# Optimization experiments

Measured on AMD Instinct MI355X. Metric: run time of the kernel, lower is better.

## Reference

```python
import jax, jax.numpy as jnp
import numpy as np

E = 16          # ensemble_size
S = 64          # state_size
A = 32          # action_size
R = 1           # reward_size
I = S + A       # combined input size
HS = 64         # SubModel_state hidden
HR = 32         # SubModel_reward hidden
B = 16384       # batch


def setup_inputs() -> dict:
    key = jax.random.key(0)
    ks = jax.random.split(key, 10)

    def init_lin(k, fan_in, shape):
        bound = 1.0 / np.sqrt(fan_in)
        return jax.random.uniform(k, shape, jnp.float32, -bound, bound)

    return {
        "state": jax.random.normal(ks[0], (B, S), jnp.float32),
        "action": jax.random.normal(ks[1], (B, A), jnp.float32),
        # stacked ensemble state-model weights (torch Linear stores [out,in]; we use [in,out])
        "W1": init_lin(ks[2], I, (E, I, HS)),
        "b1": init_lin(ks[3], I, (E, HS)),
        "W2": init_lin(ks[4], HS, (E, HS, S)),
        "b2": init_lin(ks[5], HS, (E, S)),
        # stacked ensemble reward-model weights
        "rW1": init_lin(ks[6], I, (E, I, HR)),
        "rb1": init_lin(ks[7], I, (E, HR)),
        "rW2": init_lin(ks[8], HR, (E, HR, R)),
        "rb2": init_lin(ks[9], HR, (E, R)),
    }


def reference(state, action, W1, b1, W2, b2, rW1, rb1, rW2, rb2):
    x = jnp.concatenate([state, action], axis=1)  # [B, I]
    # state models: Linear -> ReLU -> Linear, all ensemble members in one batched GEMM
    h = jax.nn.relu(jnp.einsum("bi,eih->ebh", x, W1) + b1[:, None, :])  # [E, B, HS]
    pred_states = jnp.einsum("ebh,ehs->ebs", h, W2) + b2[:, None, :]    # [E, B, S]
    # reward models: Linear -> ReLU -> Linear -> clamp(-100, 200)
    hr = jax.nn.relu(jnp.einsum("bi,eih->ebh", x, rW1) + rb1[:, None, :])  # [E, B, HR]
    pred_rewards = jnp.einsum("ebh,ehr->ebr", hr, rW2) + rb2[:, None, :]   # [E, B, R]
    pred_rewards = jnp.clip(pred_rewards, -100.0, 200.0)
    return (pred_states, pred_rewards)
```

## Files before the change

kernel.cpp:

```cpp
#include <hip/hip_runtime.h>
#include <hip/hip_bf16.h>
#include <cstdint>
#include <cstddef>

#define Bsz 16384
#define Esz 16
#define Ssz 64
#define Asz 32
#define Isz 96
#define HSz 64
#define HRz 32

#define NTM 256
#define CHUNK 512
#define NTILE 8
#define NCHUNK 32

typedef __attribute__((ext_vector_type(8))) short bf16x8;
typedef __attribute__((ext_vector_type(4))) short short4v;
typedef __attribute__((ext_vector_type(4))) float f32x4;

static __device__ __forceinline__ short f2bf(float f) {
    __hip_bfloat16 b = __float2bfloat16(f);
    return *reinterpret_cast<short*>(&b);
}
static __device__ __forceinline__ float bf2f(short s) {
    union { uint32_t u; float f; } v; v.u = ((uint32_t)(uint16_t)s) << 16; return v.f;
}
static __device__ __forceinline__ bf16x8 pack8(float4 lo, float4 hi) {
    bf16x8 r;
    r[0] = f2bf(lo.x); r[1] = f2bf(lo.y); r[2] = f2bf(lo.z); r[3] = f2bf(lo.w);
    r[4] = f2bf(hi.x); r[5] = f2bf(hi.y); r[6] = f2bf(hi.z); r[7] = f2bf(hi.w);
    return r;
}

__global__ __launch_bounds__(NTM, 2)
void fused_all(const float* __restrict__ state, const float* __restrict__ action,
               const float* __restrict__ W1, const float* __restrict__ b1,
               const float* __restrict__ W2, const float* __restrict__ b2,
               const float* __restrict__ rW1, const float* __restrict__ rb1,
               const float* __restrict__ rW2, const float* __restrict__ rb2,
               float* __restrict__ outS, float* __restrict__ outR)
{
    __shared__ __align__(16) short HT[4][16][68];

    const int bid = blockIdx.x;
    const int xcd = bid & 7;
    const int rem = bid >> 3;
    const int e   = rem & (Esz - 1);
    const int c0  = (xcd + 8 * (rem >> 4)) * CHUNK;

    const int w = threadIdx.x >> 6, lane = threadIdx.x & 63;
    const int lr = lane & 15, lg = lane >> 4;

    bf16x8 w1r[4][3], rw1r[2][3], w2r[4][2];
    {
        const float* base = W1 + (size_t)e * Isz * HSz;
        #pragma unroll
        for (int nt = 0; nt < 4; ++nt)
            #pragma unroll
            for (int kk = 0; kk < 3; ++kk) {
                const float* p = base + (kk * 32 + lg * 8) * HSz + nt * 16 + lr;
                bf16x8 r;
                #pragma unroll
                for (int t = 0; t < 8; ++t) r[t] = f2bf(p[t * HSz]);
                w1r[nt][kk] = r;
            }
    }
    {
        const float* base = rW1 + (size_t)e * Isz * HRz;
        #pragma unroll
        for (int nt = 0; nt < 2; ++nt)
            #pragma unroll
            for (int kk = 0; kk < 3; ++kk) {
                const float* p = base + (kk * 32 + lg * 8) * HRz + nt * 16 + lr;
                bf16x8 r;
                #pragma unroll
                for (int t = 0; t < 8; ++t) r[t] = f2bf(p[t * HRz]);
                rw1r[nt][kk] = r;
            }
    }
    {
        const float* base = W2 + (size_t)e * HSz * Ssz;
        #pragma unroll
        for (int nt = 0; nt < 4; ++nt)
            #pragma unroll
            for (int kk = 0; kk < 2; ++kk) {
                const float* p = base + (kk * 32 + lg * 8) * Ssz + nt * 16 + lr;
                bf16x8 r;
                #pragma unroll
                for (int t = 0; t < 8; ++t) r[t] = f2bf(p[t * Ssz]);
                w2r[nt][kk] = r;
            }
    }

    short4v b1p[4], b2p[4], rb1p[2], rw2p[2];
    #pragma unroll
    for (int nt = 0; nt < 4; ++nt) {
        float4 v1 = *(const float4*)&b1[e * HSz + nt * 16 + lg * 4];
        float4 v2 = *(const float4*)&b2[e * Ssz + nt * 16 + lg * 4];
        b1p[nt] = (short4v){ f2bf(v1.x), f2bf(v1.y), f2bf(v1.z), f2bf(v1.w) };
        b2p[nt] = (short4v){ f2bf(v2.x), f2bf(v2.y), f2bf(v2.z), f2bf(v2.w) };
    }
    #pragma unroll
    for (int nt = 0; nt < 2; ++nt) {
        float4 v1 = *(const float4*)&rb1[e * HRz + nt * 16 + lg * 4];
        float4 v2 = *(const float4*)&rW2[e * HRz + nt * 16 + lg * 4];
        rb1p[nt] = (short4v){ f2bf(v1.x), f2bf(v1.y), f2bf(v1.z), f2bf(v1.w) };
        rw2p[nt] = (short4v){ f2bf(v2.x), f2bf(v2.y), f2bf(v2.z), f2bf(v2.w) };
    }
    const float rb2s = rb2[e];

    const int row0 = c0 + w * 16 + lr;
    const float* sbase = state  + (size_t)row0 * Ssz + lg * 8;
    const float* abase = action + (size_t)row0 * Asz + lg * 8;

    float4 xs0 = *(const float4*)(sbase);
    float4 xs1 = *(const float4*)(sbase + 4);
    float4 xs2 = *(const float4*)(sbase + 32);
    float4 xs3 = *(const float4*)(sbase + 36);
    float4 xa0 = *(const float4*)(abase);
    float4 xa1 = *(const float4*)(abase + 4);
    bf16x8 a0 = pack8(xs0, xs1);
    bf16x8 a1 = pack8(xs2, xs3);
    bf16x8 a2 = pack8(xa0, xa1);

    #pragma unroll 1
    for (int t = 0; t < NTILE; ++t) {
        const int tn = (t + 1) & (NTILE - 1);
        const float* sp = sbase + (size_t)tn * 64 * Ssz;
        const float* ap = abase + (size_t)tn * 64 * Asz;
        float4 ns0 = *(const float4*)(sp);
        float4 ns1 = *(const float4*)(sp + 4);
        float4 ns2 = *(const float4*)(sp + 32);
        float4 ns3 = *(const float4*)(sp + 36);
        float4 na0 = *(const float4*)(ap);
        float4 na1 = *(const float4*)(ap + 4);

        f32x4 accS[4];
        #pragma unroll
        for (int nt = 0; nt < 4; ++nt) {
            f32x4 acc = (f32x4){ bf2f(b1p[nt][0]), bf2f(b1p[nt][1]),
                                 bf2f(b1p[nt][2]), bf2f(b1p[nt][3]) };
            acc = __builtin_amdgcn_mfma_f32_16x16x32_bf16(w1r[nt][0], a0, acc, 0, 0, 0);
            acc = __builtin_amdgcn_mfma_f32_16x16x32_bf16(w1r[nt][1], a1, acc, 0, 0, 0);
            acc = __builtin_amdgcn_mfma_f32_16x16x32_bf16(w1r[nt][2], a2, acc, 0, 0, 0);
            accS[nt] = acc;
        }
        f32x4 accR[2];
        #pragma unroll
        for (int nt = 0; nt < 2; ++nt) {
            f32x4 acc = (f32x4){ bf2f(rb1p[nt][0]), bf2f(rb1p[nt][1]),
                                 bf2f(rb1p[nt][2]), bf2f(rb1p[nt][3]) };
            acc = __builtin_amdgcn_mfma_f32_16x16x32_bf16(rw1r[nt][0], a0, acc, 0, 0, 0);
            acc = __builtin_amdgcn_mfma_f32_16x16x32_bf16(rw1r[nt][1], a1, acc, 0, 0, 0);
            acc = __builtin_amdgcn_mfma_f32_16x16x32_bf16(rw1r[nt][2], a2, acc, 0, 0, 0);
            accR[nt] = acc;
        }

        #pragma unroll
        for (int nt = 0; nt < 4; ++nt) {
            short4v p = { f2bf(fmaxf(accS[nt][0], 0.f)),
                          f2bf(fmaxf(accS[nt][1], 0.f)),
                          f2bf(fmaxf(accS[nt][2], 0.f)),
                          f2bf(fmaxf(accS[nt][3], 0.f)) };
            *(short4v*)&HT[w][lr][nt * 16 + lg * 4] = p;
        }

        float rp = 0.f;
        #pragma unroll
        for (int nt = 0; nt < 2; ++nt) {
            rp += fmaxf(accR[nt][0], 0.f) * bf2f(rw2p[nt][0]);
            rp += fmaxf(accR[nt][1], 0.f) * bf2f(rw2p[nt][1]);
            rp += fmaxf(accR[nt][2], 0.f) * bf2f(rw2p[nt][2]);
            rp += fmaxf(accR[nt][3], 0.f) * bf2f(rw2p[nt][3]);
        }
        rp += __shfl_xor(rp, 16);
        rp += __shfl_xor(rp, 32);
        if (lane < 16)
            outR[(size_t)e * Bsz + row0 + t * 64] = fminf(fmaxf(rp + rb2s, -100.f), 200.f);

        bf16x8 h0 = *(const bf16x8*)&HT[w][lr][lg * 8];
        bf16x8 h1 = *(const bf16x8*)&HT[w][lr][32 + lg * 8];
        #pragma unroll
        for (int nt = 0; nt < 4; ++nt) {
            f32x4 acc = (f32x4){ bf2f(b2p[nt][0]), bf2f(b2p[nt][1]),
                                 bf2f(b2p[nt][2]), bf2f(b2p[nt][3]) };
            acc = __builtin_amdgcn_mfma_f32_16x16x32_bf16(w2r[nt][0], h0, acc, 0, 0, 0);
            acc = __builtin_amdgcn_mfma_f32_16x16x32_bf16(w2r[nt][1], h1, acc, 0, 0, 0);
            float4 o = { acc[0], acc[1], acc[2], acc[3] };
            *(float4*)&outS[((size_t)e * Bsz + row0 + t * 64) * Ssz + nt * 16 + lg * 4] = o;
        }

        a0 = pack8(ns0, ns1);
        a1 = pack8(ns2, ns3);
        a2 = pack8(na0, na1);
    }
}

extern "C" void kernel_launch(void* const* d_in, const int* in_sizes, int n_in,
                              void* d_out, int out_size, void* d_ws, size_t ws_size,
                              hipStream_t stream) {
    const float* state  = (const float*)d_in[0];
    const float* action = (const float*)d_in[1];
    const float* W1  = (const float*)d_in[2];
    const float* b1  = (const float*)d_in[3];
    const float* W2  = (const float*)d_in[4];
    const float* b2  = (const float*)d_in[5];
    const float* rW1 = (const float*)d_in[6];
    const float* rb1 = (const float*)d_in[7];
    const float* rW2 = (const float*)d_in[8];
    const float* rb2 = (const float*)d_in[9];

    float* outS = (float*)d_out;
    float* outR = outS + (size_t)Esz * Bsz * Ssz;

    fused_all<<<Esz * (Bsz / CHUNK), NTM, 0, stream>>>(
        state, action, W1, b1, W2, b2, rW1, rb1, rW2, rb2, outS, outR);
}
```

Before: 29.13 us.

## Split state and reward models into separate block roles to cut register pressure

Each block now runs either the state MLP or the reward MLP. The grid has 512 state blocks plus 256 reward blocks, each reward block covering 1024 rows. Separating the roles lowers per-thread register demand, and launch bounds rise to 3 blocks per CU to raise occupancy. The cost is that reward blocks re-read state and action inputs from memory that the fused version shared, and the grid gains extra blocks.

```diff
diff --git a/kernel.cpp b/kernel.cpp
--- a/kernel.cpp
+++ b/kernel.cpp
@@ -12,9 +12,12 @@
 #define HRz 32
 
 #define NTM 256
-#define CHUNK 512
-#define NTILE 8
-#define NCHUNK 32
+#define SCHUNK 512
+#define SNTILE 8
+#define NSB 512
+#define RCHUNK 1024
+#define RNTILE 16
+#define NRB 256
 
 typedef __attribute__((ext_vector_type(8))) short bf16x8;
 typedef __attribute__((ext_vector_type(4))) short short4v;
@@ -34,7 +37,7 @@
     return r;
 }
 
-__global__ __launch_bounds__(NTM, 2)
+__global__ __launch_bounds__(NTM, 3)
 void fused_all(const float* __restrict__ state, const float* __restrict__ action,
                const float* __restrict__ W1, const float* __restrict__ b1,
                const float* __restrict__ W2, const float* __restrict__ b2,
@@ -45,156 +48,193 @@
     __shared__ __align__(16) short HT[4][16][68];
 
     const int bid = blockIdx.x;
-    const int xcd = bid & 7;
-    const int rem = bid >> 3;
-    const int e   = rem & (Esz - 1);
-    const int c0  = (xcd + 8 * (rem >> 4)) * CHUNK;
-
     const int w = threadIdx.x >> 6, lane = threadIdx.x & 63;
     const int lr = lane & 15, lg = lane >> 4;
 
-    bf16x8 w1r[4][3], rw1r[2][3], w2r[4][2];
-    {
-        const float* base = W1 + (size_t)e * Isz * HSz;
-        #pragma unroll
-        for (int nt = 0; nt < 4; ++nt)
-            #pragma unroll
-            for (int kk = 0; kk < 3; ++kk) {
-                const float* p = base + (kk * 32 + lg * 8) * HSz + nt * 16 + lr;
-                bf16x8 r;
+    if (bid < NSB) {
+        const int xcd = bid & 7;
+        const int rem = bid >> 3;
+        const int e   = rem & (Esz - 1);
+        const int c0  = (xcd + 8 * (rem >> 4)) * SCHUNK;
+
+        bf16x8 w1r[4][3], w2r[4][2];
+        {
+            const float* base = W1 + (size_t)e * Isz * HSz;
+            #pragma unroll
+            for (int nt = 0; nt < 4; ++nt)
                 #pragma unroll
-                for (int t = 0; t < 8; ++t) r[t] = f2bf(p[t * HSz]);
-                w1r[nt][kk] = r;
-            }
-    }
-    {
-        const float* base = rW1 + (size_t)e * Isz * HRz;
-        #pragma unroll
-        for (int nt = 0; nt < 2; ++nt)
-            #pragma unroll
-            for (int kk = 0; kk < 3; ++kk) {
-                const float* p = base + (kk * 32 + lg * 8) * HRz + nt * 16 + lr;
-                bf16x8 r;
+                for (int kk = 0; kk < 3; ++kk) {
+                    const float* p = base + (kk * 32 + lg * 8) * HSz + nt * 16 + lr;
+                    bf16x8 r;
+                    #pragma unroll
+                    for (int t = 0; t < 8; ++t) r[t] = f2bf(p[t * HSz]);
+                    w1r[nt][kk] = r;
+                }
+        }
+        {
+            const float* base = W2 + (size_t)e * HSz * Ssz;
+            #pragma unroll
+            for (int nt = 0; nt < 4; ++nt)
                 #pragma unroll
-                for (int t = 0; t < 8; ++t) r[t] = f2bf(p[t * HRz]);
-                rw1r[nt][kk] = r;
-            }
-    }
-    {
-        const float* base = W2 + (size_t)e * HSz * Ssz;
-        #pragma unroll
-        for (int nt = 0; nt < 4; ++nt)
-            #pragma unroll
-            for (int kk = 0; kk < 2; ++kk) {
-                const float* p = base + (kk * 32 + lg * 8) * Ssz + nt * 16 + lr;
-                bf16x8 r;
-                #pragma unroll
-                for (int t = 0; t < 8; ++t) r[t] = f2bf(p[t * Ssz]);
-                w2r[nt][kk] = r;
-            }
-    }
-
-    short4v b1p[4], b2p[4], rb1p[2], rw2p[2];
-    #pragma unroll
-    for (int nt = 0; nt < 4; ++nt) {
-        float4 v1 = *(const float4*)&b1[e * HSz + nt * 16 + lg * 4];
-        float4 v2 = *(const float4*)&b2[e * Ssz + nt * 16 + lg * 4];
-        b1p[nt] = (short4v){ f2bf(v1.x), f2bf(v1.y), f2bf(v1.z), f2bf(v1.w) };
-        b2p[nt] = (short4v){ f2bf(v2.x), f2bf(v2.y), f2bf(v2.z), f2bf(v2.w) };
-    }
-    #pragma unroll
-    for (int nt = 0; nt < 2; ++nt) {
-        float4 v1 = *(const float4*)&rb1[e * HRz + nt * 16 + lg * 4];
-        float4 v2 = *(const float4*)&rW2[e * HRz + nt * 16 + lg * 4];
-        rb1p[nt] = (short4v){ f2bf(v1.x), f2bf(v1.y), f2bf(v1.z), f2bf(v1.w) };
-        rw2p[nt] = (short4v){ f2bf(v2.x), f2bf(v2.y), f2bf(v2.z), f2bf(v2.w) };
-    }
-    const float rb2s = rb2[e];
-
-    const int row0 = c0 + w * 16 + lr;
-    const float* sbase = state  + (size_t)row0 * Ssz + lg * 8;
-    const float* abase = action + (size_t)row0 * Asz + lg * 8;
-
-    float4 xs0 = *(const float4*)(sbase);
-    float4 xs1 = *(const float4*)(sbase + 4);
-    float4 xs2 = *(const float4*)(sbase + 32);
-    float4 xs3 = *(const float4*)(sbase + 36);
-    float4 xa0 = *(const float4*)(abase);
-    float4 xa1 = *(const float4*)(abase + 4);
-    bf16x8 a0 = pack8(xs0, xs1);
-    bf16x8 a1 = pack8(xs2, xs3);
-    bf16x8 a2 = pack8(xa0, xa1);
-
-    #pragma unroll 1
-    for (int t = 0; t < NTILE; ++t) {
-        const int tn = (t + 1) & (NTILE - 1);
-        const float* sp = sbase + (size_t)tn * 64 * Ssz;
-        const float* ap = abase + (size_t)tn * 64 * Asz;
-        float4 ns0 = *(const float4*)(sp);
-        float4 ns1 = *(const float4*)(sp + 4);
-        float4 ns2 = *(const float4*)(sp + 32);
-        float4 ns3 = *(const float4*)(sp + 36);
-        float4 na0 = *(const float4*)(ap);
-        float4 na1 = *(const float4*)(ap + 4);
-
-        f32x4 accS[4];
+                for (int kk = 0; kk < 2; ++kk) {
+                    const float* p = base + (kk * 32 + lg * 8) * Ssz + nt * 16 + lr;
+                    bf16x8 r;
+                    #pragma unroll
+                    for (int t = 0; t < 8; ++t) r[t] = f2bf(p[t * Ssz]);
+                    w2r[nt][kk] = r;
+                }
+        }
+        short4v b1p[4], b2p[4];
         #pragma unroll
         for (int nt = 0; nt < 4; ++nt) {
-            f32x4 acc = (f32x4){ bf2f(b1p[nt][0]), bf2f(b1p[nt][1]),
-                                 bf2f(b1p[nt][2]), bf2f(b1p[nt][3]) };
-            acc = __builtin_amdgcn_mfma_f32_16x16x32_bf16(w1r[nt][0], a0, acc, 0, 0, 0);
-            acc = __builtin_amdgcn_mfma_f32_16x16x32_bf16(w1r[nt][1], a1, acc, 0, 0, 0);
-            acc = __builtin_amdgcn_mfma_f32_16x16x32_bf16(w1r[nt][2], a2, acc, 0, 0, 0);
-            accS[nt] = acc;
-        }
-        f32x4 accR[2];
+            float4 v1 = *(const float4*)&b1[e * HSz + nt * 16 + lg * 4];
+            float4 v2 = *(const float4*)&b2[e * Ssz + nt * 16 + lg * 4];
+            b1p[nt] = (short4v){ f2bf(v1.x), f2bf(v1.y), f2bf(v1.z), f2bf(v1.w) };
+            b2p[nt] = (short4v){ f2bf(v2.x), f2bf(v2.y), f2bf(v2.z), f2bf(v2.w) };
+        }
+
+        const int row0 = c0 + w * 16 + lr;
+        const float* sbase = state  + (size_t)row0 * Ssz + lg * 8;
+        const float* abase = action + (size_t)row0 * Asz + lg * 8;
+
+        float4 xs0 = *(const float4*)(sbase);
+        float4 xs1 = *(const float4*)(sbase + 4);
+        float4 xs2 = *(const float4*)(sbase + 32);
+        float4 xs3 = *(const float4*)(sbase + 36);
+        float4 xa0 = *(const float4*)(abase);
+        float4 xa1 = *(const float4*)(abase + 4);
+        bf16x8 a0 = pack8(xs0, xs1);
+        bf16x8 a1 = pack8(xs2, xs3);
+        bf16x8 a2 = pack8(xa0, xa1);
+
+        #pragma unroll 1
+        for (int t = 0; t < SNTILE; ++t) {
+            const int tn = (t + 1) & (SNTILE - 1);
+            const float* sp = sbase + (size_t)tn * 64 * Ssz;
+            const float* ap = abase + (size_t)tn * 64 * Asz;
+            float4 ns0 = *(const float4*)(sp);
+            float4 ns1 = *(const float4*)(sp + 4);
+            float4 ns2 = *(const float4*)(sp + 32);
+            float4 ns3 = *(const float4*)(sp + 36);
+            float4 na0 = *(const float4*)(ap);
+            float4 na1 = *(const float4*)(ap + 4);
+
+            f32x4 accS[4];
+            #pragma unroll
+            for (int nt = 0; nt < 4; ++nt) {
+                f32x4 acc = (f32x4){ bf2f(b1p[nt][0]), bf2f(b1p[nt][1]),
+                                     bf2f(b1p[nt][2]), bf2f(b1p[nt][3]) };
+                acc = __builtin_amdgcn_mfma_f32_16x16x32_bf16(w1r[nt][0], a0, acc, 0, 0, 0);
+                acc = __builtin_amdgcn_mfma_f32_16x16x32_bf16(w1r[nt][1], a1, acc, 0, 0, 0);
+                acc = __builtin_amdgcn_mfma_f32_16x16x32_bf16(w1r[nt][2], a2, acc, 0, 0, 0);
+                accS[nt] = acc;
+            }
+            #pragma unroll
+            for (int nt = 0; nt < 4; ++nt) {
+                short4v p = { f2bf(fmaxf(accS[nt][0], 0.f)),
+                              f2bf(fmaxf(accS[nt][1], 0.f)),
+                              f2bf(fmaxf(accS[nt][2], 0.f)),
+                              f2bf(fmaxf(accS[nt][3], 0.f)) };
+                *(short4v*)&HT[w][lr][nt * 16 + lg * 4] = p;
+            }
+            bf16x8 h0 = *(const bf16x8*)&HT[w][lr][lg * 8];
+            bf16x8 h1 = *(const bf16x8*)&HT[w][lr][32 + lg * 8];
+            #pragma unroll
+            for (int nt = 0; nt < 4; ++nt) {
+                f32x4 acc = (f32x4){ bf2f(b2p[nt][0]), bf2f(b2p[nt][1]),
+                                     bf2f(b2p[nt][2]), bf2f(b2p[nt][3]) };
+                acc = __builtin_amdgcn_mfma_f32_16x16x32_bf16(w2r[nt][0], h0, acc, 0, 0, 0);
+                acc = __builtin_amdgcn_mfma_f32_16x16x32_bf16(w2r[nt][1], h1, acc, 0, 0, 0);
+                float4 o = { acc[0], acc[1], acc[2], acc[3] };
+                *(float4*)&outS[((size_t)e * Bsz + row0 + t * 64) * Ssz + nt * 16 + lg * 4] = o;
+            }
+            a0 = pack8(ns0, ns1);
+            a1 = pack8(ns2, ns3);
+            a2 = pack8(na0, na1);
+        }
+    } else {
+        const int rbid = bid - NSB;
+        const int e  = rbid & (Esz - 1);
+        const int c0 = (rbid >> 4) * RCHUNK;
+
+        bf16x8 rw1r[2][3];
+        {
+            const float* base = rW1 + (size_t)e * Isz * HRz;
+            #pragma unroll
+            for (int nt = 0; nt < 2; ++nt)
+                #pragma unroll
+                for (int kk = 0; kk < 3; ++kk) {
+                    const float* p = base + (kk * 32 + lg * 8) * HRz + nt * 16 + lr;
+                    bf16x8 r;
+                    #pragma unroll
+                    for (int t = 0; t < 8; ++t) r[t] = f2bf(p[t * HRz]);
+                    rw1r[nt][kk] = r;
+                }
+        }
+        short4v rb1p[2], rw2p[2];
         #pragma unroll
         for (int nt = 0; nt < 2; ++nt) {
-            f32x4 acc = (f32x4){ bf2f(rb1p[nt][0]), bf2f(rb1p[nt][1]),
-                                 bf2f(rb1p[nt][2]), bf2f(rb1p[nt][3]) };
-            acc = __builtin_amdgcn_mfma_f32_16x16x32_bf16(rw1r[nt][0], a0, acc, 0, 0, 0);
-            acc = __builtin_amdgcn_mfma_f32_16x16x32_bf16(rw1r[nt][1], a1, acc, 0, 0, 0);
-            acc = __builtin_amdgcn_mfma_f32_16x16x32_bf16(rw1r[nt][2], a2, acc, 0, 0, 0);
-            accR[nt] = acc;
-        }
-
-        #pragma unroll
-        for (int nt = 0; nt < 4; ++nt) {
-            short4v p = { f2bf(fmaxf(accS[nt][0], 0.f)),
-                          f2bf(fmaxf(accS[nt][1], 0.f)),
-                          f2bf(fmaxf(accS[nt][2], 0.f)),
-                          f2bf(fmaxf(accS[nt][3], 0.f)) };
-            *(short4v*)&HT[w][lr][nt * 16 + lg * 4] = p;
-        }
-
-        float rp = 0.f;
-        #pragma unroll
-        for (int nt = 0; nt < 2; ++nt) {
-            rp += fmaxf(accR[nt][0], 0.f) * bf2f(rw2p[nt][0]);
-            rp += fmaxf(accR[nt][1], 0.f) * bf2f(rw2p[nt][1]);
-            rp += fmaxf(accR[nt][2], 0.f) * bf2f(rw2p[nt][2]);
-            rp += fmaxf(accR[nt][3], 0.f) * bf2f(rw2p[nt][3]);
-        }
-        rp += __shfl_xor(rp, 16);
-        rp += __shfl_xor(rp, 32);
-        if (lane < 16)
-            outR[(size_t)e * Bsz + row0 + t * 64] = fminf(fmaxf(rp + rb2s, -100.f), 200.f);
-
-        bf16x8 h0 = *(const bf16x8*)&HT[w][lr][lg * 8];
-        bf16x8 h1 = *(const bf16x8*)&HT[w][lr][32 + lg * 8];
-        #pragma unroll
-        for (int nt = 0; nt < 4; ++nt) {
-            f32x4 acc = (f32x4){ bf2f(b2p[nt][0]), bf2f(b2p[nt][1]),
-                                 bf2f(b2p[nt][2]), bf2f(b2p[nt][3]) };
-            acc = __builtin_amdgcn_mfma_f32_16x16x32_bf16(w2r[nt][0], h0, acc, 0, 0, 0);
-            acc = __builtin_amdgcn_mfma_f32_16x16x32_bf16(w2r[nt][1], h1, acc, 0, 0, 0);
-            float4 o = { acc[0], acc[1], acc[2], acc[3] };
-            *(float4*)&outS[((size_t)e * Bsz + row0 + t * 64) * Ssz + nt * 16 + lg * 4] = o;
-        }
-
-        a0 = pack8(ns0, ns1);
-        a1 = pack8(ns2, ns3);
-        a2 = pack8(na0, na1);
+            float4 v1 = *(const float4*)&rb1[e * HRz + nt * 16 + lg * 4];
+            float4 v2 = *(const float4*)&rW2[e * HRz + nt * 16 + lg * 4];
+            rb1p[nt] = (short4v){ f2bf(v1.x), f2bf(v1.y), f2bf(v1.z), f2bf(v1.w) };
+            rw2p[nt] = (short4v){ f2bf(v2.x), f2bf(v2.y), f2bf(v2.z), f2bf(v2.w) };
+        }
+        const float rb2s = rb2[e];
+
+        const int row0 = c0 + w * 16 + lr;
+        const float* sbase = state  + (size_t)row0 * Ssz + lg * 8;
+        const float* abase = action + (size_t)row0 * Asz + lg * 8;
+
+        float4 xs0 = *(const float4*)(sbase);
+        float4 xs1 = *(const float4*)(sbase + 4);
+        float4 xs2 = *(const float4*)(sbase + 32);
+        float4 xs3 = *(const float4*)(sbase + 36);
+        float4 xa0 = *(const float4*)(abase);
+        float4 xa1 = *(const float4*)(abase + 4);
+        bf16x8 a0 = pack8(xs0, xs1);
+        bf16x8 a1 = pack8(xs2, xs3);
+        bf16x8 a2 = pack8(xa0, xa1);
+
+        #pragma unroll 1
+        for (int t = 0; t < RNTILE; ++t) {
+            const int tn = (t + 1) & (RNTILE - 1);
+            const float* sp = sbase + (size_t)tn * 64 * Ssz;
+            const float* ap = abase + (size_t)tn * 64 * Asz;
+            float4 ns0 = *(const float4*)(sp);
+            float4 ns1 = *(const float4*)(sp + 4);
+            float4 ns2 = *(const float4*)(sp + 32);
+            float4 ns3 = *(const float4*)(sp + 36);
+            float4 na0 = *(const float4*)(ap);
+            float4 na1 = *(const float4*)(ap + 4);
+
+            f32x4 accR[2];
+            #pragma unroll
+            for (int nt = 0; nt < 2; ++nt) {
+                f32x4 acc = (f32x4){ bf2f(rb1p[nt][0]), bf2f(rb1p[nt][1]),
+                                     bf2f(rb1p[nt][2]), bf2f(rb1p[nt][3]) };
+                acc = __builtin_amdgcn_mfma_f32_16x16x32_bf16(rw1r[nt][0], a0, acc, 0, 0, 0);
+                acc = __builtin_amdgcn_mfma_f32_16x16x32_bf16(rw1r[nt][1], a1, acc, 0, 0, 0);
+                acc = __builtin_amdgcn_mfma_f32_16x16x32_bf16(rw1r[nt][2], a2, acc, 0, 0, 0);
+                accR[nt] = acc;
+            }
+            float rp = 0.f;
+            #pragma unroll
+            for (int nt = 0; nt < 2; ++nt) {
+                rp += fmaxf(accR[nt][0], 0.f) * bf2f(rw2p[nt][0]);
+                rp += fmaxf(accR[nt][1], 0.f) * bf2f(rw2p[nt][1]);
+                rp += fmaxf(accR[nt][2], 0.f) * bf2f(rw2p[nt][2]);
+                rp += fmaxf(accR[nt][3], 0.f) * bf2f(rw2p[nt][3]);
+            }
+            rp += __shfl_xor(rp, 16);
+            rp += __shfl_xor(rp, 32);
+            if (lane < 16)
+                outR[(size_t)e * Bsz + row0 + t * 64] =
+                    fminf(fmaxf(rp + rb2s, -100.f), 200.f);
+
+            a0 = pack8(ns0, ns1);
+            a1 = pack8(ns2, ns3);
+            a2 = pack8(na0, na1);
+        }
     }
 }
 
@@ -215,6 +255,6 @@
     float* outS = (float*)d_out;
     float* outR = outS + (size_t)Esz * Bsz * Ssz;
 
-    fused_all<<<Esz * (Bsz / CHUNK), NTM, 0, stream>>>(
+    fused_all<<<NSB + NRB, NTM, 0, stream>>>(
         state, action, W1, b1, W2, b2, rW1, rb1, rW2, rb2, outS, outR);
 }
```

After: 39.40 us. 35.3% more time.
